# Kernel tuning notes

Measured on AMD Instinct MI355X. Metric: run time of the kernel, lower is better.

## Reference

```python
import jax, jax.numpy as jnp
import numpy as np

SEQ, BATCH, IN_DIM, HID = 512, 128, 1024, 1024

def setup_inputs() -> dict:
    key = jax.random.key(0)
    k1, k2, k3, k4 = jax.random.split(key, 4)
    scale = 0.02  # keep gate pre-activations in a sane range
    return {
        "inputs": jax.random.normal(k1, (SEQ, BATCH, IN_DIM), dtype=jnp.float32),
        "proj_W": jax.random.normal(k2, (4 * HID, IN_DIM + HID), dtype=jnp.float32) * scale,
        "proj_b": jax.random.normal(k3, (4 * HID,), dtype=jnp.float32) * scale,
        "qgate_W": jax.random.normal(k4, (HID, HID), dtype=jnp.float32) * scale,
    }

def reference(inputs, proj_W, proj_b, qgate_W):
    # inputs: [S, B, I]; proj_W: [4H, I+H]; qgate_W: [H, H]
    S, B, I = inputs.shape
    H = qgate_W.shape[0]
    Wx = proj_W[:, :I]   # [4H, I]
    Wh = proj_W[:, I:]   # [4H, H]
    # Precompute the input part of proj(cat([x, hx])) for all timesteps (same math).
    x_proj = jnp.einsum('sbi,gi->sbg', inputs, Wx) + proj_b  # [S, B, 4H]

    qWt = qgate_W.T
    def qgate(z):
        return jax.nn.sigmoid(z @ qWt)

    def step(carry, xp):
        hx, cx = carry
        gates = xp + hx @ Wh.T  # [B, 4H]
        f_in, i_in, g_in, o_in = jnp.split(gates, 4, axis=-1)
        # mixed/quantum mode: shared quantum gate, then outer nonlinearity (sigmoid of sigmoid, tanh of sigmoid)
        f = jax.nn.sigmoid(qgate(f_in))
        i = jax.nn.sigmoid(qgate(i_in))
        g = jnp.tanh(qgate(g_in))
        o = jax.nn.sigmoid(qgate(o_in))
        cx = f * cx + i * g
        hx = o * jnp.tanh(cx)
        return (hx, cx), hx

    init = (jnp.zeros((B, H), inputs.dtype), jnp.zeros((B, H), inputs.dtype))
    (hx, cx), outs = jax.lax.scan(step, init, x_proj)
    return outs, hx, cx
```

## Files before the change

kernel.cpp:

```cpp
#include <hip/hip_runtime.h>

typedef unsigned short ushort_t;
typedef __attribute__((ext_vector_type(4))) float f32x4;
typedef __attribute__((ext_vector_type(8))) __bf16 bf16x8;

#define SEQ   512
#define BATCH 128
#define HID   1024
#define G4    4096
#define CHUNK 64
#define BH    (BATCH*HID)
#define NBLK  256
#define FLAG_STRIDE 32
#define SCAN_LDS (131072 + 32768)
#define GEMM256_LDS 131072

__device__ __forceinline__ ushort_t f2bf(float f) {
  unsigned u = __float_as_uint(f);
  u += 0x7FFFu + ((u >> 16) & 1u);
  return (ushort_t)(u >> 16);
}
__device__ __forceinline__ float bf2f(ushort_t h) {
  return __uint_as_float(((unsigned)h) << 16);
}
__device__ __forceinline__ float sigm(float x) { return 1.0f / (1.0f + __expf(-x)); }
__device__ __forceinline__ float ftanh(float x) {
  float xc = fminf(fmaxf(x, -15.f), 15.f);
  float t = __expf(2.f * xc);
  return (t - 1.f) / (t + 1.f);
}

__device__ __forceinline__ void lds16(const ushort_t* g, ushort_t* l) {
  __builtin_amdgcn_global_load_lds(
      (const __attribute__((address_space(1))) unsigned int*)g,
      (__attribute__((address_space(3))) unsigned int*)l, 16, 0, 0);
}
__device__ __forceinline__ void lds16c(const ushort_t* g, ushort_t* l) {
  __builtin_amdgcn_global_load_lds(
      (const __attribute__((address_space(1))) unsigned int*)g,
      (__attribute__((address_space(3))) unsigned int*)l, 16, 0, 0x11);
}

__global__ void cast_f32_bf16(const float* __restrict__ in, ushort_t* __restrict__ out, int n4) {
  int i = blockIdx.x * blockDim.x + threadIdx.x;
  if (i < n4) {
    float4 v = ((const float4*)in)[i];
    union { ushort_t u[4]; uint2 v2; } o;
    o.u[0] = f2bf(v.x); o.u[1] = f2bf(v.y); o.u[2] = f2bf(v.z); o.u[3] = f2bf(v.w);
    ((uint2*)out)[i] = o.v2;
  }
}

__global__ __launch_bounds__(256) void transpose_cast(const float* __restrict__ pw, ushort_t* __restrict__ pwt) {
  __shared__ float tile[32][33];
  int bx = blockIdx.x, by = blockIdx.y;
  int tx = threadIdx.x & 31, ty = threadIdx.x >> 5;
  for (int i = 0; i < 32; i += 8)
    tile[ty + i][tx] = pw[(size_t)(by*32 + ty + i)*2048 + bx*32 + tx];
  __syncthreads();
  for (int i = 0; i < 32; i += 8) {
    int r = ty + i;
    pwt[(size_t)(bx*32 + r)*4096 + by*32 + tx] = f2bf(tile[tx][r]);
  }
}

__global__ void bias_fold(const float* __restrict__ qW, const float* __restrict__ pb, float* __restrict__ b2) {
  int r = blockIdx.x;
  int j = r & (HID-1), gb = r & ~(HID-1);
  float s = 0.f;
  for (int k = threadIdx.x; k < HID; k += 64)
    s += qW[(size_t)j*HID + k] * pb[gb + k];
  for (int off = 32; off; off >>= 1) s += __shfl_down(s, off, 64);
  if (threadIdx.x == 0) b2[r] = s;
}

__global__ __launch_bounds__(256) void gemm128(
    const ushort_t* __restrict__ A, int lda, unsigned arow_mask,
    const ushort_t* __restrict__ B, int ldb, unsigned bko_mask,
    const float* __restrict__ bias, ushort_t* __restrict__ C, int ldc, int K)
{
  __shared__ __align__(16) ushort_t Al[128*64];
  __shared__ __align__(16) ushort_t Bl[128*64];
  const int tid = threadIdx.x, wv = tid >> 6, ln = tid & 63;
  const int bn = blockIdx.x, bm = blockIdx.y;
  const int bko = (int)(((unsigned)(bm << 7)) & bko_mask);
  const int m0 = (wv & 1) << 6, n0 = (wv >> 1) << 6;
  f32x4 acc[4][4] = {};
  for (int k0 = 0; k0 < K; k0 += 64) {
    for (int rr = 0; rr < 4; ++rr) {
      int r0 = (rr << 5) + (wv << 3);
      unsigned ga = ((unsigned)((bm << 7) + r0 + (ln >> 3))) & arow_mask;
      lds16(A + (size_t)ga*lda + k0 + ((ln & 7) << 3), &Al[r0 << 6]);
      unsigned gbr = (unsigned)((bn << 7) + r0 + (ln >> 3));
      lds16(B + (size_t)gbr*ldb + bko + k0 + ((ln & 7) << 3), &Bl[r0 << 6]);
    }
    __syncthreads();
    for (int kk = 0; kk < 64; kk += 32) {
      const int lrow = ln & 15, lk = kk + ((ln >> 4) << 3);
      bf16x8 af[4], bfr[4];
      for (int i = 0; i < 4; ++i) af[i]  = *(const bf16x8*)&Al[((m0 + (i << 4) + lrow) << 6) + lk];
      for (int j = 0; j < 4; ++j) bfr[j] = *(const bf16x8*)&Bl[((n0 + (j << 4) + lrow) << 6) + lk];
      for (int i = 0; i < 4; ++i)
        for (int j = 0; j < 4; ++j)
          acc[i][j] = __builtin_amdgcn_mfma_f32_16x16x32_bf16(af[i], bfr[j], acc[i][j], 0, 0, 0);
    }
    __syncthreads();
  }
  for (int i = 0; i < 4; ++i)
    for (int j = 0; j < 4; ++j) {
      int col = (bn << 7) + n0 + (j << 4) + (ln & 15);
      float bv = bias ? bias[col] : 0.f;
      for (int r = 0; r < 4; ++r) {
        int row = (bm << 7) + m0 + (i << 4) + ((ln >> 4) << 2) + r;
        C[(size_t)row*ldc + col] = f2bf(acc[i][j][r] + bv);
      }
    }
}

__global__ __launch_bounds__(512) void gemm256(
    const ushort_t* __restrict__ A, const ushort_t* __restrict__ B,
    const float* __restrict__ bias, ushort_t* __restrict__ C)
{
  extern __shared__ __align__(16) ushort_t lds[];
  ushort_t* LA = lds;
  ushort_t* LB = lds + 32768;
  const int tid = threadIdx.x, wv8 = tid >> 6, ln = tid & 63;
  const int wm = wv8 >> 2, wn = wv8 & 3;
  const int bn = blockIdx.x, bm = blockIdx.y;
  const int lr = ln & 15, lg = ln >> 4;

  f32x4 acc[8][4] = {};
  bf16x8 af[4][2], bfr[4][2];

  auto stA = [&](int db, int half, int kt) {
    ushort_t* d = LA + db*16384 + half*8192 + (wv8 << 9);
    const int ce = ((ln & 7) ^ (ln >> 3)) << 3;
    #pragma unroll
    for (int p = 0; p < 2; ++p) {
      int rr = half*128 + p*64 + (wv8 << 3) + (ln >> 3);
      lds16(A + (size_t)(bm*256 + rr)*1024 + kt*64 + ce, d + p*4096);
    }
  };
  auto stB = [&](int db, int half, int kt) {
    ushort_t* d = LB + db*16384 + half*8192 + (wv8 << 9);
    const int ce = ((ln & 7) ^ (ln >> 3)) << 3;
    #pragma unroll
    for (int p = 0; p < 2; ++p) {
      int rr = half*128 + p*64 + (wv8 << 3) + (ln >> 3);
      lds16(B + (size_t)(bn*256 + rr)*2048 + kt*64 + ce, d + p*4096);
    }
  };

#define RD_A(DB, MQ) { _Pragma("unroll") for (int i_ = 0; i_ < 4; ++i_) { \
    const int row_ = ((MQ)*4 + i_)*16 + lr; \
    const ushort_t* b_ = &LA[(DB)*16384 + wm*8192 + row_*64]; \
    af[i_][0] = *(const bf16x8*)&b_[ (lg << 3)       ^ ((lr & 7) << 3)]; \
    af[i_][1] = *(const bf16x8*)&b_[((lg << 3) | 32) ^ ((lr & 7) << 3)]; } }

#define RD_B(DB, NQ) { _Pragma("unroll") for (int j_ = 0; j_ < 2; ++j_) { \
    const int row_ = (wn & 1)*64 + ((NQ)*2 + j_)*16 + lr; \
    const ushort_t* b_ = &LB[(DB)*16384 + (wn >> 1)*8192 + row_*64]; \
    bfr[(NQ)*2 + j_][0] = *(const bf16x8*)&b_[ (lg << 3)       ^ ((lr & 7) << 3)]; \
    bfr[(NQ)*2 + j_][1] = *(const bf16x8*)&b_[((lg << 3) | 32) ^ ((lr & 7) << 3)]; } }

#define QUAD(MQ, NQ) \
  __builtin_amdgcn_s_setprio(1); \
  { _Pragma("unroll") for (int i_ = 0; i_ < 4; ++i_) \
      _Pragma("unroll") for (int j_ = 0; j_ < 2; ++j_) \
        _Pragma("unroll") for (int k_ = 0; k_ < 2; ++k_) \
          acc[(MQ)*4 + i_][(NQ)*2 + j_] = __builtin_amdgcn_mfma_f32_16x16x32_bf16( \
              af[i_][k_], bfr[(NQ)*2 + j_][k_], acc[(MQ)*4 + i_][(NQ)*2 + j_], 0, 0, 0); } \
  __builtin_amdgcn_s_setprio(0);

#define BAR() __builtin_amdgcn_s_barrier()
#define LGK0() do { asm volatile("s_waitcnt lgkmcnt(0)" ::: "memory"); \
                    __builtin_amdgcn_sched_barrier(0); } while (0)
#define VM4() do { asm volatile("s_waitcnt vmcnt(4)" ::: "memory"); \
                   __builtin_amdgcn_sched_barrier(0); } while (0)

  stA(0,0,0); stA(0,1,0); stB(0,0,0); stB(0,1,0); stB(1,0,1); stB(1,1,1);
  asm volatile("s_waitcnt vmcnt(4)" ::: "memory");
  BAR();

  for (int i = 0; i < 8; ++i) {
    const int k1 = 2*i + 1, k2 = 2*i + 2, k3 = 2*i + 3;
    RD_A(0,0); RD_B(0,0); stA(1,0,k1);            BAR(); LGK0(); QUAD(0,0); BAR();
    RD_B(0,1); stA(1,1,k1);                       BAR(); LGK0(); QUAD(0,1); BAR();
    RD_A(0,1); if (k2 < 16) stB(0,0,k2);          BAR(); LGK0(); QUAD(1,0); BAR();
    if (k2 < 16) stB(0,1,k2);                     BAR();         QUAD(1,1); VM4(); BAR();
    RD_A(1,0); RD_B(1,0); if (k2 < 16) stA(0,0,k2); BAR(); LGK0(); QUAD(0,0); BAR();
    RD_B(1,1); if (k2 < 16) stA(0,1,k2);          BAR(); LGK0(); QUAD(0,1); BAR();
    RD_A(1,1); if (k3 < 16) stB(1,0,k3);          BAR(); LGK0(); QUAD(1,0); BAR();
    if (k3 < 16) stB(1,1,k3);                     BAR();         QUAD(1,1); VM4(); BAR();
  }

  const int crow0 = bm*256 + wm*128;
  const int ccol0 = bn*256 + wn*64;
  #pragma unroll
  for (int m = 0; m < 8; ++m)
    #pragma unroll
    for (int n = 0; n < 4; ++n) {
      int col = ccol0 + n*16 + lr;
      float bv = bias[col];
      #pragma unroll
      for (int r = 0; r < 4; ++r) {
        int row = crow0 + m*16 + lg*4 + r;
        C[(size_t)row*4096 + col] = f2bf(acc[m][n][r] + bv);
      }
    }
#undef RD_A
#undef RD_B
#undef QUAD
#undef BAR
#undef LGK0
#undef VM4
}

__global__ __launch_bounds__(256, 1) void qlstm_scan(
    const ushort_t* __restrict__ P,
    const ushort_t* __restrict__ W2,
    ushort_t* __restrict__ hxb,
    float* __restrict__ cxg,
    float* __restrict__ outc,
    int t0,
    unsigned* __restrict__ flags)
{
  extern __shared__ __align__(16) ushort_t lds[];
  ushort_t* Ul = lds;
  ushort_t* Ar = lds + 65536;
  float*    sm = (float*)(lds + 65536);

  const int tid = threadIdx.x, wv = tid >> 6, ln = tid & 63;
  const int rblk = blockIdx.x & 3, cblk = blockIdx.x >> 2;
  unsigned* gflags = flags + (size_t)rblk*64*FLAG_STRIDE;

  for (int ck = 0; ck < 8; ++ck)
    for (int rr = 0; rr < 4; ++rr) {
      int lr = rr*16 + wv*4 + (ln >> 4);
      int grow = ((lr >> 4) << 10) + cblk*16 + (lr & 15);
      int gcol = ck*128 + (((ln & 15) ^ (lr & 7)) << 3);
      lds16(W2 + (size_t)grow*2048 + 1024 + gcol, &Ul[ck*8192 + (rr*16 + wv*4)*128]);
    }

  const int b_loc = tid >> 3;
  const int j0    = (tid & 7) << 1;
  const size_t ci = (size_t)(rblk*32 + b_loc)*1024 + cblk*16 + j0;
  float2 cxr = *(const float2*)&cxg[ci];

  auto stageA = [&](int slot, int k0, const ushort_t* hxR) {
    #pragma unroll
    for (int rr = 0; rr < 2; ++rr) {
      int row = rr*16 + wv*4 + (ln >> 4);
      int gcol = ((ln & 15) ^ (row & 7)) << 3;
      lds16c(hxR + (size_t)(rblk*32 + row)*1024 + k0 + gcol,
             &Ar[slot*4096 + (rr*16 + wv*4)*128]);
    }
  };
  auto load_pv = [&](int tl, float* pv) {
    #pragma unroll
    for (int i = 0; i < 2; ++i)
      #pragma unroll
      for (int r = 0; r < 4; ++r) {
        int bl = i*16 + ((ln >> 4) << 2) + r;
        pv[i*4+r] = bf2f(P[(size_t)(tl*128 + rblk*32 + bl)*4096 + (wv << 10) + cblk*16 + (ln & 15)]);
      }
  };

  float pv[8];
  load_pv(0, pv);

  for (int tl = 0; tl < CHUNK; ++tl) {
    const int t = t0 + tl;
    const ushort_t* hxR = hxb + (size_t)(t % 3)*BH;
    ushort_t*       hxW = hxb + (size_t)((t + 1) % 3)*BH;

    f32x4 acc0 = {}, acc1 = {};
    stageA(0, 0, hxR);
    stageA(1, 128, hxR);
    stageA(2, 256, hxR);

    #define COMPUTE_CK(CK)                                                         \
      {                                                                            \
        const int aslot = (CK) & 3;                                                \
        _Pragma("unroll")                                                          \
        for (int k4 = 0; k4 < 4; ++k4) {                                           \
          int s = k4*4 + (ln >> 4);                                                \
          int ar0 = ln & 15, ar1 = 16 + (ln & 15);                                 \
          int brow = wv*16 + (ln & 15);                                            \
          bf16x8 a0 = *(const bf16x8*)&Ar[aslot*4096 + ar0*128 + ((s ^ (ar0 & 7)) << 3)]; \
          bf16x8 a1 = *(const bf16x8*)&Ar[aslot*4096 + ar1*128 + ((s ^ (ar1 & 7)) << 3)]; \
          bf16x8 bb = *(const bf16x8*)&Ul[(CK)*8192 + brow*128 + ((s ^ (brow & 7)) << 3)]; \
          acc0 = __builtin_amdgcn_mfma_f32_16x16x32_bf16(a0, bb, acc0, 0, 0, 0);   \
          acc1 = __builtin_amdgcn_mfma_f32_16x16x32_bf16(a1, bb, acc1, 0, 0, 0);   \
        }                                                                          \
      }
    #define STEP_CK(CK, WN, DOSTAGE)                                               \
      asm volatile("s_waitcnt vmcnt(" #WN ")" ::: "memory");                       \
      __builtin_amdgcn_s_barrier();                                                \
      if (DOSTAGE) stageA(((CK)+3) & 3, ((CK)+3)*128, hxR);                        \
      COMPUTE_CK(CK)

    STEP_CK(0, 4, 1) STEP_CK(1, 4, 1) STEP_CK(2, 4, 1)
    STEP_CK(3, 4, 1) STEP_CK(4, 4, 1)
    STEP_CK(5, 4, 0) STEP_CK(6, 2, 0) STEP_CK(7, 0, 0)
    #undef STEP_CK
    #undef COMPUTE_CK

    #pragma unroll
    for (int i = 0; i < 2; ++i)
      #pragma unroll
      for (int r = 0; r < 4; ++r) {
        int bl = i*16 + ((ln >> 4) << 2) + r;
        float v = (i ? acc1[r] : acc0[r]) + pv[i*4+r];
        sm[wv*512 + bl*16 + (ln & 15)] = sigm(v);
      }
    __syncthreads();
    float2 h2;
    {
      const float2* sm2 = (const float2*)sm;
      int e = b_loc*8 + (j0 >> 1);
      float2 sF = sm2[0*256 + e], sI = sm2[1*256 + e];
      float2 sG = sm2[2*256 + e], sO = sm2[3*256 + e];
      float f0 = sigm(sF.x), i0 = sigm(sI.x), g0 = ftanh(sG.x), o0 = sigm(sO.x);
      float f1 = sigm(sF.y), i1 = sigm(sI.y), g1 = ftanh(sG.y), o1 = sigm(sO.y);
      float cn0 = f0*cxr.x + i0*g0, cn1 = f1*cxr.y + i1*g1;
      float h0 = o0*ftanh(cn0),     h1 = o1*ftanh(cn1);
      cxr.x = cn0; cxr.y = cn1;
      h2.x = h0; h2.y = h1;
      unsigned hp = (unsigned)f2bf(h0) | ((unsigned)f2bf(h1) << 16);
      __hip_atomic_store((unsigned*)&hxW[ci], hp,
                         __ATOMIC_RELAXED, __HIP_MEMORY_SCOPE_AGENT);
    }

    if (tl != CHUNK - 1) {
      const unsigned gen = (unsigned)(t + 1);
      asm volatile("s_waitcnt vmcnt(0)" ::: "memory");
      __syncthreads();
      if (tid == 0)
        __hip_atomic_store(gflags + (size_t)cblk*FLAG_STRIDE, gen,
                           __ATOMIC_RELAXED, __HIP_MEMORY_SCOPE_AGENT);
      *(float2*)&outc[(size_t)tl*BH + ci] = h2;
      float pvn[8];
      load_pv(tl + 1, pvn);
      if (tid < 64) {
        int it = 0;
        for (;;) {
          unsigned a = __hip_atomic_load(gflags + (size_t)tid*FLAG_STRIDE,
                                         __ATOMIC_RELAXED, __HIP_MEMORY_SCOPE_AGENT);
          if (__all(a >= gen)) break;
          if ((++it & 255) == 0) __builtin_amdgcn_fence(__ATOMIC_ACQUIRE, "agent");
          __builtin_amdgcn_s_sleep(1);
        }
      }
      __syncthreads();
      #pragma unroll
      for (int q = 0; q < 8; ++q) pv[q] = pvn[q];
    } else {
      *(float2*)&outc[(size_t)tl*BH + ci] = h2;
    }
  }
  *(float2*)&cxg[ci] = cxr;
}

extern "C" void kernel_launch(void* const* d_in, const int* in_sizes, int n_in,
                              void* d_out, int out_size, void* d_ws, size_t ws_size,
                              hipStream_t stream) {
  const float* x  = (const float*)d_in[0];
  const float* pW = (const float*)d_in[1];
  const float* pb = (const float*)d_in[2];
  const float* qW = (const float*)d_in[3];
  float* out = (float*)d_out;

  char* w = (char*)d_ws;
  auto carve = [&](size_t bytes) { char* p = w; w += (bytes + 255) & ~(size_t)255; return p; };
  ushort_t* qWbf = (ushort_t*)carve((size_t)HID*HID*2);
  ushort_t* pWt  = (ushort_t*)carve((size_t)2048*4096*2);
  ushort_t* W2   = (ushort_t*)carve((size_t)4096*2048*2);
  float*    b2   = (float*)   carve((size_t)4096*4);
  ushort_t* hxb  = (ushort_t*)carve((size_t)3*BH*2);
  float*    cxws = (float*)   carve((size_t)BH*4);
  unsigned* flags= (unsigned*)carve((size_t)NBLK*FLAG_STRIDE*4);
  ushort_t* xbf  = (ushort_t*)carve((size_t)CHUNK*BATCH*HID*2);
  ushort_t* Pc   = (ushort_t*)carve((size_t)CHUNK*BATCH*G4*2);

  (void)hipFuncSetAttribute((const void*)qlstm_scan,
                            hipFuncAttributeMaxDynamicSharedMemorySize, SCAN_LDS);
  (void)hipFuncSetAttribute((const void*)gemm256,
                            hipFuncAttributeMaxDynamicSharedMemorySize, GEMM256_LDS);

  cast_f32_bf16<<<(HID*HID/4 + 255)/256, 256, 0, stream>>>(qW, qWbf, HID*HID/4);
  transpose_cast<<<dim3(64, 128), 256, 0, stream>>>(pW, pWt);
  bias_fold<<<4096, 64, 0, stream>>>(qW, pb, b2);
  gemm128<<<dim3(16, 32), 256, 0, stream>>>(qWbf, 1024, 1023u, pWt, 4096, ~1023u, nullptr, W2, 2048, 1024);

  hipMemsetAsync(hxb, 0, (size_t)BH*2, stream);
  hipMemsetAsync(cxws, 0, (size_t)BH*4, stream);
  hipMemsetAsync(flags, 0, (size_t)NBLK*FLAG_STRIDE*4, stream);

  for (int c = 0; c < SEQ/CHUNK; ++c) {
    cast_f32_bf16<<<(CHUNK*BATCH*HID/4 + 255)/256, 256, 0, stream>>>(
        x + (size_t)c*CHUNK*BATCH*HID, xbf, CHUNK*BATCH*HID/4);
    gemm256<<<dim3(G4/256, CHUNK*BATCH/256), 512, GEMM256_LDS, stream>>>(
        xbf, W2, b2, Pc);

    const ushort_t* Pa = Pc; const ushort_t* W2a = W2;
    ushort_t* hxa = hxb; float* cxa = cxws;
    float* outa = out + (size_t)c*CHUNK*BH;
    int t0 = c*CHUNK; unsigned* fla = flags;
    void* args[7] = { &Pa, &W2a, &hxa, &cxa, &outa, &t0, &fla };
    hipLaunchCooperativeKernel((const void*)qlstm_scan, dim3(NBLK), dim3(256),
                               args, SCAN_LDS, stream);
  }
  hipMemcpyAsync(out + (size_t)SEQ*BH,      out + (size_t)(SEQ-1)*BH, (size_t)BH*4,
                 hipMemcpyDeviceToDevice, stream);
  hipMemcpyAsync(out + (size_t)SEQ*BH + BH, cxws, (size_t)BH*4,
                 hipMemcpyDeviceToDevice, stream);
}
```

Before: 2.995 ms.

## Split scan blocks into two independent batch streams to overlap sync waits

Each of the 256 blocks now owns 8 hidden columns and two 32-row batch groups that are processed one after the other, each with its own flag set. Synchronisation is per batch group, so a block can work on one stream while the other group's peers catch up. This halves the recurrent-weight tile in LDS, shrinking the scan kernel's shared memory, and moves the P prefetch into the k-loop. In exchange there are more flag polls per step, smaller MFMA tiles, and only half the threads take part in the elementwise cell update.

```diff
diff --git a/kernel.cpp b/kernel.cpp
--- a/kernel.cpp
+++ b/kernel.cpp
@@ -12,7 +12,7 @@
 #define BH    (BATCH*HID)
 #define NBLK  256
 #define FLAG_STRIDE 32
-#define SCAN_LDS (131072 + 32768)
+#define SCAN_LDS 131072
 #define GEMM256_LDS 131072
 
 __device__ __forceinline__ ushort_t f2bf(float f) {
@@ -216,6 +216,95 @@
 #undef VM4
 }
 
+__device__ __forceinline__ void stream_step(
+    ushort_t* __restrict__ Ar, float* __restrict__ sm,
+    const ushort_t* __restrict__ Ul,
+    const ushort_t* __restrict__ hxR, ushort_t* __restrict__ hxW,
+    int rbase, unsigned* __restrict__ fl,
+    const ushort_t* __restrict__ Pt,
+    int pcol, float2& cx, size_t ci, float* __restrict__ outt,
+    unsigned t, int wv, int ln, int tid, int cblk8)
+{
+  const int rh = wv & 1, uh = wv >> 1;
+  const int lr15 = ln & 15, lg = ln >> 4;
+
+  for (;;) {
+    unsigned a = __hip_atomic_load(fl + (size_t)ln*FLAG_STRIDE,
+                                   __ATOMIC_RELAXED, __HIP_MEMORY_SCOPE_AGENT);
+    unsigned b = __hip_atomic_load(fl + (size_t)(64 + ln)*FLAG_STRIDE,
+                                   __ATOMIC_RELAXED, __HIP_MEMORY_SCOPE_AGENT);
+    if (__all(a >= t && b >= t)) break;
+    __builtin_amdgcn_s_sleep(1);
+  }
+
+  auto stg = [&](int slot, int k0) {
+    #pragma unroll
+    for (int rr = 0; rr < 2; ++rr) {
+      int row = rr*16 + wv*4 + (ln >> 4);
+      int gcol = ((ln & 15) ^ (row & 7)) << 3;
+      lds16c(hxR + (size_t)(rbase + row)*1024 + k0 + gcol,
+             &Ar[slot*4096 + (rr*16 + wv*4)*128]);
+    }
+  };
+  f32x4 acc = {};
+  stg(0, 0); stg(1, 128); stg(2, 256);
+  const int ar = rh*16 + lr15, ur = uh*16 + lr15;
+  ushort_t pv0, pv1, pv2, pv3;
+
+#define CCK(CK) { _Pragma("unroll") for (int k4 = 0; k4 < 4; ++k4) { \
+    int s = k4*4 + lg; \
+    bf16x8 av = *(const bf16x8*)&Ar[((CK)&3)*4096 + ar*128 + ((s ^ (ar & 7)) << 3)]; \
+    bf16x8 bv = *(const bf16x8*)&Ul[(CK)*4096 + ur*128 + ((s ^ (ur & 7)) << 3)]; \
+    acc = __builtin_amdgcn_mfma_f32_16x16x32_bf16(av, bv, acc, 0, 0, 0); } }
+#define SCK(CK, WN, DS) \
+  asm volatile("s_waitcnt vmcnt(" #WN ")" ::: "memory"); \
+  __builtin_amdgcn_s_barrier(); \
+  if (DS) stg(((CK)+3)&3, ((CK)+3)*128); \
+  CCK(CK)
+
+  SCK(0,4,1) SCK(1,4,1) SCK(2,4,1) SCK(3,4,1) SCK(4,4,1)
+  SCK(5,4,0)
+  {
+    const int rb = rh*16 + lg*4;
+    pv0 = Pt[(size_t)(rb + 0)*4096 + pcol];
+    pv1 = Pt[(size_t)(rb + 1)*4096 + pcol];
+    pv2 = Pt[(size_t)(rb + 2)*4096 + pcol];
+    pv3 = Pt[(size_t)(rb + 3)*4096 + pcol];
+  }
+  SCK(6,10,0) SCK(7,8,0)
+#undef SCK
+#undef CCK
+
+  {
+    int base = (uh*2 + (lr15 >> 3))*256 + (rh*16 + lg*4)*8 + (lr15 & 7);
+    sm[base +  0] = sigm(acc[0] + bf2f(pv0));
+    sm[base +  8] = sigm(acc[1] + bf2f(pv1));
+    sm[base + 16] = sigm(acc[2] + bf2f(pv2));
+    sm[base + 24] = sigm(acc[3] + bf2f(pv3));
+  }
+  __syncthreads();
+  float2 h2;
+  if (tid < 128) {
+    int b0 = (tid >> 2)*8 + (tid & 3)*2;
+    float f0 = sigm(sm[b0]),       f1 = sigm(sm[b0 + 1]);
+    float i0 = sigm(sm[256 + b0]), i1 = sigm(sm[256 + b0 + 1]);
+    float g0 = ftanh(sm[512 + b0]), g1 = ftanh(sm[512 + b0 + 1]);
+    float o0 = sigm(sm[768 + b0]), o1 = sigm(sm[768 + b0 + 1]);
+    float cn0 = f0*cx.x + i0*g0, cn1 = f1*cx.y + i1*g1;
+    float h0 = o0*ftanh(cn0),    h1 = o1*ftanh(cn1);
+    cx.x = cn0; cx.y = cn1; h2.x = h0; h2.y = h1;
+    unsigned hp = (unsigned)f2bf(h0) | ((unsigned)f2bf(h1) << 16);
+    __hip_atomic_store((unsigned*)&hxW[ci], hp,
+                       __ATOMIC_RELAXED, __HIP_MEMORY_SCOPE_AGENT);
+  }
+  asm volatile("s_waitcnt vmcnt(0)" ::: "memory");
+  __syncthreads();
+  if (tid == 0)
+    __hip_atomic_store(fl + (size_t)cblk8*FLAG_STRIDE, t + 1,
+                       __ATOMIC_RELAXED, __HIP_MEMORY_SCOPE_AGENT);
+  if (tid < 128) *(float2*)&outt[ci] = h2;
+}
+
 __global__ __launch_bounds__(256, 1) void qlstm_scan(
     const ushort_t* __restrict__ P,
     const ushort_t* __restrict__ W2,
@@ -226,140 +315,59 @@
     unsigned* __restrict__ flags)
 {
   extern __shared__ __align__(16) ushort_t lds[];
-  ushort_t* Ul = lds;
-  ushort_t* Ar = lds + 65536;
-  float*    sm = (float*)(lds + 65536);
+  ushort_t* Ul  = lds;
+  ushort_t* ArA = lds + 32768;
+  ushort_t* ArB = lds + 49152;
+  float* smA = (float*)ArA;
+  float* smB = (float*)ArB;
 
   const int tid = threadIdx.x, wv = tid >> 6, ln = tid & 63;
-  const int rblk = blockIdx.x & 3, cblk = blockIdx.x >> 2;
-  unsigned* gflags = flags + (size_t)rblk*64*FLAG_STRIDE;
+  const int pr = blockIdx.x & 1, cblk8 = blockIdx.x >> 1;
+  const int rA = 2*pr, rB = 2*pr + 1;
+  const int uh = wv >> 1, lr15 = ln & 15;
 
   for (int ck = 0; ck < 8; ++ck)
-    for (int rr = 0; rr < 4; ++rr) {
-      int lr = rr*16 + wv*4 + (ln >> 4);
-      int grow = ((lr >> 4) << 10) + cblk*16 + (lr & 15);
-      int gcol = ck*128 + (((ln & 15) ^ (lr & 7)) << 3);
-      lds16(W2 + (size_t)grow*2048 + 1024 + gcol, &Ul[ck*8192 + (rr*16 + wv*4)*128]);
-    }
-
-  const int b_loc = tid >> 3;
-  const int j0    = (tid & 7) << 1;
-  const size_t ci = (size_t)(rblk*32 + b_loc)*1024 + cblk*16 + j0;
-  float2 cxr = *(const float2*)&cxg[ci];
-
-  auto stageA = [&](int slot, int k0, const ushort_t* hxR) {
     #pragma unroll
     for (int rr = 0; rr < 2; ++rr) {
-      int row = rr*16 + wv*4 + (ln >> 4);
-      int gcol = ((ln & 15) ^ (row & 7)) << 3;
-      lds16c(hxR + (size_t)(rblk*32 + row)*1024 + k0 + gcol,
-             &Ar[slot*4096 + (rr*16 + wv*4)*128]);
-    }
-  };
-  auto load_pv = [&](int tl, float* pv) {
-    #pragma unroll
-    for (int i = 0; i < 2; ++i)
-      #pragma unroll
-      for (int r = 0; r < 4; ++r) {
-        int bl = i*16 + ((ln >> 4) << 2) + r;
-        pv[i*4+r] = bf2f(P[(size_t)(tl*128 + rblk*32 + bl)*4096 + (wv << 10) + cblk*16 + (ln & 15)]);
-      }
-  };
-
-  float pv[8];
-  load_pv(0, pv);
+      int lrr = rr*16 + wv*4 + (ln >> 4);
+      int grow = (lrr >> 3)*1024 + cblk8*8 + (lrr & 7);
+      int gcol = ck*128 + (((ln & 15) ^ (lrr & 7)) << 3);
+      lds16(W2 + (size_t)grow*2048 + 1024 + gcol, &Ul[ck*4096 + (rr*16 + wv*4)*128]);
+    }
+
+  size_t ciA = 0, ciB = 0;
+  float2 cxA; cxA.x = 0.f; cxA.y = 0.f;
+  float2 cxB; cxB.x = 0.f; cxB.y = 0.f;
+  if (tid < 128) {
+    int erow = tid >> 2, ec = (tid & 3)*2;
+    ciA = (size_t)(rA*32 + erow)*1024 + cblk8*8 + ec;
+    ciB = (size_t)(rB*32 + erow)*1024 + cblk8*8 + ec;
+    cxA = *(const float2*)&cxg[ciA];
+    cxB = *(const float2*)&cxg[ciB];
+  }
+  unsigned* flA = flags + (size_t)rA*128*FLAG_STRIDE;
+  unsigned* flB = flags + (size_t)rB*128*FLAG_STRIDE;
+  const int pcol = (uh*2 + (lr15 >> 3))*1024 + cblk8*8 + (lr15 & 7);
+
+  asm volatile("s_waitcnt vmcnt(0)" ::: "memory");
+  __syncthreads();
 
   for (int tl = 0; tl < CHUNK; ++tl) {
     const int t = t0 + tl;
     const ushort_t* hxR = hxb + (size_t)(t % 3)*BH;
     ushort_t*       hxW = hxb + (size_t)((t + 1) % 3)*BH;
-
-    f32x4 acc0 = {}, acc1 = {};
-    stageA(0, 0, hxR);
-    stageA(1, 128, hxR);
-    stageA(2, 256, hxR);
-
-    #define COMPUTE_CK(CK)                                                         \
-      {                                                                            \
-        const int aslot = (CK) & 3;                                                \
-        _Pragma("unroll")                                                          \
-        for (int k4 = 0; k4 < 4; ++k4) {                                           \
-          int s = k4*4 + (ln >> 4);                                                \
-          int ar0 = ln & 15, ar1 = 16 + (ln & 15);                                 \
-          int brow = wv*16 + (ln & 15);                                            \
-          bf16x8 a0 = *(const bf16x8*)&Ar[aslot*4096 + ar0*128 + ((s ^ (ar0 & 7)) << 3)]; \
-          bf16x8 a1 = *(const bf16x8*)&Ar[aslot*4096 + ar1*128 + ((s ^ (ar1 & 7)) << 3)]; \
-          bf16x8 bb = *(const bf16x8*)&Ul[(CK)*8192 + brow*128 + ((s ^ (brow & 7)) << 3)]; \
-          acc0 = __builtin_amdgcn_mfma_f32_16x16x32_bf16(a0, bb, acc0, 0, 0, 0);   \
-          acc1 = __builtin_amdgcn_mfma_f32_16x16x32_bf16(a1, bb, acc1, 0, 0, 0);   \
-        }                                                                          \
-      }
-    #define STEP_CK(CK, WN, DOSTAGE)                                               \
-      asm volatile("s_waitcnt vmcnt(" #WN ")" ::: "memory");                       \
-      __builtin_amdgcn_s_barrier();                                                \
-      if (DOSTAGE) stageA(((CK)+3) & 3, ((CK)+3)*128, hxR);                        \
-      COMPUTE_CK(CK)
-
-    STEP_CK(0, 4, 1) STEP_CK(1, 4, 1) STEP_CK(2, 4, 1)
-    STEP_CK(3, 4, 1) STEP_CK(4, 4, 1)
-    STEP_CK(5, 4, 0) STEP_CK(6, 2, 0) STEP_CK(7, 0, 0)
-    #undef STEP_CK
-    #undef COMPUTE_CK
-
-    #pragma unroll
-    for (int i = 0; i < 2; ++i)
-      #pragma unroll
-      for (int r = 0; r < 4; ++r) {
-        int bl = i*16 + ((ln >> 4) << 2) + r;
-        float v = (i ? acc1[r] : acc0[r]) + pv[i*4+r];
-        sm[wv*512 + bl*16 + (ln & 15)] = sigm(v);
-      }
-    __syncthreads();
-    float2 h2;
-    {
-      const float2* sm2 = (const float2*)sm;
-      int e = b_loc*8 + (j0 >> 1);
-      float2 sF = sm2[0*256 + e], sI = sm2[1*256 + e];
-      float2 sG = sm2[2*256 + e], sO = sm2[3*256 + e];
-      float f0 = sigm(sF.x), i0 = sigm(sI.x), g0 = ftanh(sG.x), o0 = sigm(sO.x);
-      float f1 = sigm(sF.y), i1 = sigm(sI.y), g1 = ftanh(sG.y), o1 = sigm(sO.y);
-      float cn0 = f0*cxr.x + i0*g0, cn1 = f1*cxr.y + i1*g1;
-      float h0 = o0*ftanh(cn0),     h1 = o1*ftanh(cn1);
-      cxr.x = cn0; cxr.y = cn1;
-      h2.x = h0; h2.y = h1;
-      unsigned hp = (unsigned)f2bf(h0) | ((unsigned)f2bf(h1) << 16);
-      __hip_atomic_store((unsigned*)&hxW[ci], hp,
-                         __ATOMIC_RELAXED, __HIP_MEMORY_SCOPE_AGENT);
-    }
-
-    if (tl != CHUNK - 1) {
-      const unsigned gen = (unsigned)(t + 1);
-      asm volatile("s_waitcnt vmcnt(0)" ::: "memory");
-      __syncthreads();
-      if (tid == 0)
-        __hip_atomic_store(gflags + (size_t)cblk*FLAG_STRIDE, gen,
-                           __ATOMIC_RELAXED, __HIP_MEMORY_SCOPE_AGENT);
-      *(float2*)&outc[(size_t)tl*BH + ci] = h2;
-      float pvn[8];
-      load_pv(tl + 1, pvn);
-      if (tid < 64) {
-        int it = 0;
-        for (;;) {
-          unsigned a = __hip_atomic_load(gflags + (size_t)tid*FLAG_STRIDE,
-                                         __ATOMIC_RELAXED, __HIP_MEMORY_SCOPE_AGENT);
-          if (__all(a >= gen)) break;
-          if ((++it & 255) == 0) __builtin_amdgcn_fence(__ATOMIC_ACQUIRE, "agent");
-          __builtin_amdgcn_s_sleep(1);
-        }
-      }
-      __syncthreads();
-      #pragma unroll
-      for (int q = 0; q < 8; ++q) pv[q] = pvn[q];
-    } else {
-      *(float2*)&outc[(size_t)tl*BH + ci] = h2;
-    }
-  }
-  *(float2*)&cxg[ci] = cxr;
+    float* outt = outc + (size_t)tl*BH;
+    stream_step(ArA, smA, Ul, hxR, hxW, rA*32, flA,
+                P + (size_t)(tl*128 + rA*32)*4096, pcol,
+                cxA, ciA, outt, (unsigned)t, wv, ln, tid, cblk8);
+    stream_step(ArB, smB, Ul, hxR, hxW, rB*32, flB,
+                P + (size_t)(tl*128 + rB*32)*4096, pcol,
+                cxB, ciB, outt, (unsigned)t, wv, ln, tid, cblk8);
+  }
+  if (tid < 128) {
+    *(float2*)&cxg[ciA] = cxA;
+    *(float2*)&cxg[ciB] = cxB;
+  }
 }
 
 extern "C" void kernel_launch(void* const* d_in, const int* in_sizes, int n_in,
@@ -379,7 +387,7 @@
   float*    b2   = (float*)   carve((size_t)4096*4);
   ushort_t* hxb  = (ushort_t*)carve((size_t)3*BH*2);
   float*    cxws = (float*)   carve((size_t)BH*4);
-  unsigned* flags= (unsigned*)carve((size_t)NBLK*FLAG_STRIDE*4);
+  unsigned* flags= (unsigned*)carve((size_t)4*128*FLAG_STRIDE*4);
   ushort_t* xbf  = (ushort_t*)carve((size_t)CHUNK*BATCH*HID*2);
   ushort_t* Pc   = (ushort_t*)carve((size_t)CHUNK*BATCH*G4*2);
 
@@ -395,7 +403,7 @@
 
   hipMemsetAsync(hxb, 0, (size_t)BH*2, stream);
   hipMemsetAsync(cxws, 0, (size_t)BH*4, stream);
-  hipMemsetAsync(flags, 0, (size_t)NBLK*FLAG_STRIDE*4, stream);
+  hipMemsetAsync(flags, 0, (size_t)4*128*FLAG_STRIDE*4, stream);
 
   for (int c = 0; c < SEQ/CHUNK; ++c) {
     cast_f32_bf16<<<(CHUNK*BATCH*HID/4 + 255)/256, 256, 0, stream>>>(
```

Result: slower. 4.408 ms (+47.2%).
